# Performance work log

Measured on AMD Instinct MI355X. Metric: run time of the kernel, lower is better.

Reference implementation:

```python
import jax, jax.numpy as jnp
import numpy as np

IN_SIZE = 1024
CLASSES = 7
N = 50000
LN_EPS = 1e-5


def _chain(x, w, b, g, beta):
    # Linear -> (Dropout=identity at eval) -> LayerNorm -> GELU(exact erf)
    h = x @ w.T + b
    mu = jnp.mean(h, axis=-1, keepdims=True)
    var = jnp.var(h, axis=-1, keepdims=True)
    h = (h - mu) / jnp.sqrt(var + LN_EPS) * g + beta
    return jax.nn.gelu(h, approximate=False)


def setup_inputs() -> dict:
    key = jax.random.key(0)
    ks = jax.random.split(key, 16)
    d = IN_SIZE
    std = 1.0 / np.sqrt(d)
    inp = {
        "features": jax.random.normal(ks[0], (N, d), jnp.float32),
        "c": jax.random.normal(ks[1], (N, CLASSES), jnp.float32),
        "key_w": jax.random.uniform(ks[2], (d, d), jnp.float32, -std, std),
        "key_b": jax.random.uniform(ks[3], (d,), jnp.float32, -std, std),
        "key_g": jnp.ones((d,), jnp.float32),
        "key_beta": jnp.zeros((d,), jnp.float32),
        "query_w": jax.random.uniform(ks[4], (d, d), jnp.float32, -std, std),
        "query_b": jax.random.uniform(ks[5], (d,), jnp.float32, -std, std),
        "query_g": jnp.ones((d,), jnp.float32),
        "query_beta": jnp.zeros((d,), jnp.float32),
        "value_w": jax.random.uniform(ks[6], (d, d), jnp.float32, -std, std),
        "value_b": jax.random.uniform(ks[7], (d,), jnp.float32, -std, std),
        "value_g": jnp.ones((d,), jnp.float32),
        "value_beta": jnp.zeros((d,), jnp.float32),
        "head_w": jax.random.uniform(ks[8], (CLASSES, CLASSES, d), jnp.float32, -1.0 / np.sqrt(CLASSES * d), 1.0 / np.sqrt(CLASSES * d)),
        "head_b": jax.random.uniform(ks[9], (CLASSES,), jnp.float32, -1.0 / np.sqrt(CLASSES * d), 1.0 / np.sqrt(CLASSES * d)),
    }
    return inp


def reference(features, c, key_w, key_b, key_g, key_beta,
              query_w, query_b, query_g, query_beta,
              value_w, value_b, value_g, value_beta,
              head_w, head_b):
    K = _chain(features, key_w, key_b, key_g, key_beta)          # [N, d]
    V = _chain(K, value_w, value_b, value_g, value_beta)         # [N, d]
    Q = _chain(K, query_w, query_b, query_g, query_beta)         # [N, d]
    # critical (top-scoring) instance per class
    top_idx = jnp.argmax(c, axis=0)                              # [classes]
    m_feats = K[top_idx]                                         # [classes, d]
    q_max = _chain(m_feats, query_w, query_b, query_g, query_beta)  # [classes, d]
    A = Q @ q_max.T                                              # [N, classes]
    A = jax.nn.softmax(A / jnp.sqrt(jnp.float32(Q.shape[1])), axis=0)
    B = A.T @ V                                                  # [classes, d]
    # Conv1d(classes, classes, kernel_size=d) on [1, classes, d] -> full contraction
    C = jnp.einsum('ik,oik->o', B, head_w) + head_b              # [classes]
    C = C.reshape(1, -1)
    return (C, A, B.reshape(1, CLASSES, -1))
```

## Files before the change

kernel.cpp:

```cpp
#include <hip/hip_runtime.h>


typedef unsigned short u16;
typedef __attribute__((ext_vector_type(8))) short          bf16x8;
typedef __attribute__((ext_vector_type(8))) unsigned short u16x8;
typedef __attribute__((ext_vector_type(4))) unsigned short u16x4;
typedef __attribute__((ext_vector_type(4))) float          f32x4;

#define DDIM  1024
#define NROWS 50000
#define MP    50048
#define NCLS  7
#define MPD4  12512

__device__ __forceinline__ u16 f2bf(float f) {
  unsigned u = __float_as_uint(f);
  u = (u + 0x7FFFu + ((u >> 16) & 1u)) >> 16;
  return (u16)u;
}
__device__ __forceinline__ float bf2f(u16 h) {
  return __uint_as_float(((unsigned)h) << 16);
}
__device__ __forceinline__ float gelu(float x) {
  return 0.5f * x * (1.0f + erff(x * 0.70710678118654752f));
}

__device__ __forceinline__ void load16_lds(const u16* g, u16* l) {
  __builtin_amdgcn_global_load_lds(
      (const __attribute__((address_space(1))) unsigned int*)(const void*)g,
      (__attribute__((address_space(3))) unsigned int*)(void*)l, 16, 0, 0);
}

__global__ __launch_bounds__(256) void k_convert(const float* __restrict__ src,
                                                 u16* __restrict__ dst,
                                                 int rows_total, int rows_valid) {
  const size_t total = (size_t)rows_total * DDIM / 8;
  const size_t stride = (size_t)gridDim.x * blockDim.x;
  for (size_t i = (size_t)blockIdx.x * blockDim.x + threadIdx.x; i < total; i += stride) {
    const size_t e = i * 8;
    const int row = (int)(e >> 10);
    u16x8 o = {0, 0, 0, 0, 0, 0, 0, 0};
    if (row < rows_valid) {
      const float4* p = (const float4*)(src + e);
      float4 f0 = p[0], f1 = p[1];
      o[0] = f2bf(f0.x); o[1] = f2bf(f0.y); o[2] = f2bf(f0.z); o[3] = f2bf(f0.w);
      o[4] = f2bf(f1.x); o[5] = f2bf(f1.y); o[6] = f2bf(f1.z); o[7] = f2bf(f1.w);
    }
    *(u16x8*)(dst + e) = o;
  }
}

__global__ __launch_bounds__(256) void k_convw(const float* __restrict__ kw,
                                               const float* __restrict__ vw,
                                               const float* __restrict__ qw,
                                               u16* __restrict__ Wk,
                                               u16* __restrict__ Wvq) {
  const int w = blockIdx.x >> 7;
  const int b = blockIdx.x & 127;
  const float* src = (w == 0) ? kw : (w == 1) ? vw : qw;
  u16* dst = (w == 0) ? Wk : (Wvq + (size_t)(w - 1) * DDIM * DDIM);
  for (int i = b * 256 + threadIdx.x; i < DDIM * DDIM / 8; i += 128 * 256) {
    const float4* p = (const float4*)(src + (size_t)i * 8);
    float4 f0 = p[0], f1 = p[1];
    u16x8 o;
    o[0] = f2bf(f0.x); o[1] = f2bf(f0.y); o[2] = f2bf(f0.z); o[3] = f2bf(f0.w);
    o[4] = f2bf(f1.x); o[5] = f2bf(f1.y); o[6] = f2bf(f1.z); o[7] = f2bf(f1.w);
    *(u16x8*)(dst + (size_t)i * 8) = o;
  }
}

__global__ __launch_bounds__(256) void k_gemm_bt(const u16* __restrict__ A,
                                                 const u16* __restrict__ B,
                                                 u16* __restrict__ C,
                                                 int lnn, int ldc) {
  __shared__ __align__(16) u16 As[3][4096];
  __shared__ __align__(16) u16 Bs[3][4096];
  const int tid  = threadIdx.x;
  const int lane = tid & 63;
  const int cpx = gridDim.x >> 3;
  const int v   = (blockIdx.x & 7) * cpx + (blockIdx.x >> 3);
  const int m0 = (v >> lnn) * 128;
  const int n0 = (v & ((1 << lnn) - 1)) * 128;
  const int wid = tid >> 6;
  const int wr = (wid >> 1) * 64;
  const int wc = (wid & 1) * 64;

  const int rA = tid >> 2;
  const int cA = (((tid & 3) ^ ((rA >> 1) & 3)) << 3);
  const u16* Ap0 = A + (size_t)(m0 + rA) * DDIM + cA;
  const u16* Ap1 = Ap0 + (size_t)64 * DDIM;
  const u16* Bp0 = B + (size_t)(n0 + rA) * DDIM + cA;
  const u16* Bp1 = Bp0 + (size_t)64 * DDIM;
  const int wb8 = wid * 512;

  f32x4 acc[4][4] = {};
  const int fr = lane & 15;
  const int T  = lane >> 4;

#define STAGE_KT(KT, BUF) do { const int _ko = (KT) * 32;                      \
    load16_lds(Ap0 + _ko, &As[BUF][wb8]);                                      \
    load16_lds(Ap1 + _ko, &As[BUF][wb8 + 2048]);                               \
    load16_lds(Bp0 + _ko, &Bs[BUF][wb8]);                                      \
    load16_lds(Bp1 + _ko, &Bs[BUF][wb8 + 2048]); } while (0)

#define COMPUTE_KT(BUF) do {                                                   \
    const u16* _Ab = &As[BUF][0]; const u16* _Bb = &Bs[BUF][0];                \
    bf16x8 a[4], b[4];                                                         \
    _Pragma("unroll") for (int i = 0; i < 4; ++i) {                            \
      const int R = wr + i * 16 + fr;                                          \
      a[i] = *(const bf16x8*)&_Ab[R * 32 + ((T ^ ((R >> 1) & 3)) << 3)];       \
    }                                                                          \
    _Pragma("unroll") for (int j = 0; j < 4; ++j) {                            \
      const int R = wc + j * 16 + fr;                                          \
      b[j] = *(const bf16x8*)&_Bb[R * 32 + ((T ^ ((R >> 1) & 3)) << 3)];       \
    }                                                                          \
    _Pragma("unroll") for (int i = 0; i < 4; ++i)                              \
      _Pragma("unroll") for (int j = 0; j < 4; ++j)                            \
        acc[i][j] = __builtin_amdgcn_mfma_f32_16x16x32_bf16(a[i], b[j],        \
                                                            acc[i][j], 0, 0, 0); } while (0)

#define RBAR(N) asm volatile("s_waitcnt vmcnt(" #N ")\n\ts_barrier" ::: "memory")

  STAGE_KT(0, 0); STAGE_KT(1, 1);
  RBAR(4);
  for (int kt = 0; kt < 30; kt += 3) {
    STAGE_KT(kt + 2, 2); COMPUTE_KT(0); RBAR(4);
    STAGE_KT(kt + 3, 0); COMPUTE_KT(1); RBAR(4);
    STAGE_KT(kt + 4, 1); COMPUTE_KT(2); RBAR(4);
  }
  COMPUTE_KT(0);
  RBAR(0);
  COMPUTE_KT(1);
#undef STAGE_KT
#undef COMPUTE_KT
#undef RBAR

  const int orow = (lane >> 4) * 4;
  const int ocol = lane & 15;
#pragma unroll
  for (int i = 0; i < 4; ++i)
#pragma unroll
    for (int j = 0; j < 4; ++j) {
      const size_t base = (size_t)(m0 + wr + i * 16 + orow) * ldc + (n0 + wc + j * 16 + ocol);
#pragma unroll
      for (int r = 0; r < 4; ++r)
        C[base + (size_t)r * ldc] = f2bf(acc[i][j][r]);
    }
}

__global__ __launch_bounds__(256) void k_ln_k(const u16* __restrict__ h,
                                              const float* __restrict__ bias,
                                              const float* __restrict__ g,
                                              const float* __restrict__ beta,
                                              u16* __restrict__ out) {
  const int lane = threadIdx.x & 63;
  const int row = blockIdx.x * 4 + (threadIdx.x >> 6);
  const int c0 = lane * 8;
  u16x8* op0 = (u16x8*)(out + (size_t)row * DDIM + c0);
  u16x8* op1 = (u16x8*)(out + (size_t)row * DDIM + 512 + c0);
  if (row >= NROWS) {
    u16x8 z = {0, 0, 0, 0, 0, 0, 0, 0};
    *op0 = z; *op1 = z;
    return;
  }
  u16x8 h0 = *(const u16x8*)(h + (size_t)row * DDIM + c0);
  u16x8 h1 = *(const u16x8*)(h + (size_t)row * DDIM + 512 + c0);
  float4 a0 = *(const float4*)(bias + c0), a1 = *(const float4*)(bias + c0 + 4);
  float4 a2 = *(const float4*)(bias + 512 + c0), a3 = *(const float4*)(bias + 512 + c0 + 4);
  const float ba[8] = {a0.x, a0.y, a0.z, a0.w, a1.x, a1.y, a1.z, a1.w};
  const float bb[8] = {a2.x, a2.y, a2.z, a2.w, a3.x, a3.y, a3.z, a3.w};
  float v0[8], v1[8];
  float s1 = 0.f, s2 = 0.f;
#pragma unroll
  for (int e = 0; e < 8; ++e) {
    v0[e] = bf2f(h0[e]) + ba[e];
    v1[e] = bf2f(h1[e]) + bb[e];
    s1 += v0[e] + v1[e];
    s2 += v0[e] * v0[e] + v1[e] * v1[e];
  }
#pragma unroll
  for (int m = 1; m < 64; m <<= 1) {
    s1 += __shfl_xor(s1, m, 64);
    s2 += __shfl_xor(s2, m, 64);
  }
  const float mu = s1 * (1.0f / 1024.0f);
  const float var = s2 * (1.0f / 1024.0f) - mu * mu;
  const float rs = rsqrtf(var + 1e-5f);
  float4 g0 = *(const float4*)(g + c0), g1 = *(const float4*)(g + c0 + 4);
  float4 g2 = *(const float4*)(g + 512 + c0), g3 = *(const float4*)(g + 512 + c0 + 4);
  float4 t0 = *(const float4*)(beta + c0), t1 = *(const float4*)(beta + c0 + 4);
  float4 t2 = *(const float4*)(beta + 512 + c0), t3 = *(const float4*)(beta + 512 + c0 + 4);
  const float ga[8] = {g0.x, g0.y, g0.z, g0.w, g1.x, g1.y, g1.z, g1.w};
  const float gb[8] = {g2.x, g2.y, g2.z, g2.w, g3.x, g3.y, g3.z, g3.w};
  const float ta[8] = {t0.x, t0.y, t0.z, t0.w, t1.x, t1.y, t1.z, t1.w};
  const float tb[8] = {t2.x, t2.y, t2.z, t2.w, t3.x, t3.y, t3.z, t3.w};
  u16x8 o0, o1;
#pragma unroll
  for (int e = 0; e < 8; ++e) {
    o0[e] = f2bf(gelu((v0[e] - mu) * rs * ga[e] + ta[e]));
    o1[e] = f2bf(gelu((v1[e] - mu) * rs * gb[e] + tb[e]));
  }
  *op0 = o0; *op1 = o1;
}

__global__ __launch_bounds__(64) void k_qmax2(const float* __restrict__ argv,
                                              const int* __restrict__ argi,
                                              const u16* __restrict__ hvq,
                                              const float* __restrict__ qb,
                                              const float* __restrict__ qg,
                                              const float* __restrict__ qbeta,
                                              u16* __restrict__ qm) {
  const int j = blockIdx.x;
  const int lane = threadIdx.x;
  float bv = -3.4e38f; int bi = 0x7fffffff;
  for (int p = lane; p < 128; p += 64) {
    const float v = argv[p * NCLS + j];
    const int   i = argi[p * NCLS + j];
    if (v > bv || (v == bv && i < bi)) { bv = v; bi = i; }
  }
#pragma unroll
  for (int m = 1; m < 64; m <<= 1) {
    const float ov = __shfl_xor(bv, m, 64);
    const int   oi = __shfl_xor(bi, m, 64);
    if (ov > bv || (ov == bv && oi < bi)) { bv = ov; bi = oi; }
  }
  const int row = bi;
  const int c0 = lane * 8;
  const u16* hp = hvq + (size_t)row * 2048 + DDIM;
  u16x8 h0 = *(const u16x8*)(hp + c0);
  u16x8 h1 = *(const u16x8*)(hp + 512 + c0);
  float v0[8], v1[8];
  float s1 = 0.f, s2 = 0.f;
#pragma unroll
  for (int e = 0; e < 8; ++e) {
    v0[e] = bf2f(h0[e]) + qb[c0 + e];
    v1[e] = bf2f(h1[e]) + qb[512 + c0 + e];
    s1 += v0[e] + v1[e];
    s2 += v0[e] * v0[e] + v1[e] * v1[e];
  }
#pragma unroll
  for (int m = 1; m < 64; m <<= 1) {
    s1 += __shfl_xor(s1, m, 64);
    s2 += __shfl_xor(s2, m, 64);
  }
  const float mu = s1 * (1.0f / 1024.0f);
  const float var = s2 * (1.0f / 1024.0f) - mu * mu;
  const float rs = rsqrtf(var + 1e-5f);
  u16x8 o0, o1;
#pragma unroll
  for (int e = 0; e < 8; ++e) {
    o0[e] = f2bf(gelu((v0[e] - mu) * rs * qg[c0 + e] + qbeta[c0 + e]));
    o1[e] = f2bf(gelu((v1[e] - mu) * rs * qg[512 + c0 + e] + qbeta[512 + c0 + e]));
  }
  *(u16x8*)(qm + (size_t)j * DDIM + c0) = o0;
  *(u16x8*)(qm + (size_t)j * DDIM + 512 + c0) = o1;
}

__global__ __launch_bounds__(256) void k_ln_vq(const u16* __restrict__ h,
                                               const float* __restrict__ v_b,
                                               const float* __restrict__ v_g,
                                               const float* __restrict__ v_beta,
                                               const float* __restrict__ q_b,
                                               const float* __restrict__ q_g,
                                               const float* __restrict__ q_beta,
                                               const u16* __restrict__ qm,
                                               u16* __restrict__ V,
                                               float* __restrict__ logits) {
  __shared__ __align__(16) u16 sqm[NCLS * DDIM];
  const int tid = threadIdx.x;
  const int lane = tid & 63;
  const int half = (blockIdx.x >= MPD4) ? 1 : 0;
  const int rb = half ? (blockIdx.x - MPD4) : blockIdx.x;
  const int row = rb * 4 + (tid >> 6);
  if (half) {
    for (int i = tid; i < NCLS * DDIM / 8; i += 256)
      *(u16x8*)&sqm[i * 8] = *(const u16x8*)&qm[i * 8];
    __syncthreads();
  }
  if (row >= NROWS) return;
  const float* bias = half ? q_b : v_b;
  const float* gain = half ? q_g : v_g;
  const float* bet  = half ? q_beta : v_beta;
  const int c0 = lane * 8;
  const u16* hp = h + (size_t)row * 2048 + (size_t)half * DDIM;
  u16x8 h0 = *(const u16x8*)(hp + c0);
  u16x8 h1 = *(const u16x8*)(hp + 512 + c0);
  float4 a0 = *(const float4*)(bias + c0), a1 = *(const float4*)(bias + c0 + 4);
  float4 a2 = *(const float4*)(bias + 512 + c0), a3 = *(const float4*)(bias + 512 + c0 + 4);
  const float ba[8] = {a0.x, a0.y, a0.z, a0.w, a1.x, a1.y, a1.z, a1.w};
  const float bb[8] = {a2.x, a2.y, a2.z, a2.w, a3.x, a3.y, a3.z, a3.w};
  float v0[8], v1[8];
  float s1 = 0.f, s2 = 0.f;
#pragma unroll
  for (int e = 0; e < 8; ++e) {
    v0[e] = bf2f(h0[e]) + ba[e];
    v1[e] = bf2f(h1[e]) + bb[e];
    s1 += v0[e] + v1[e];
    s2 += v0[e] * v0[e] + v1[e] * v1[e];
  }
#pragma unroll
  for (int m = 1; m < 64; m <<= 1) {
    s1 += __shfl_xor(s1, m, 64);
    s2 += __shfl_xor(s2, m, 64);
  }
  const float mu = s1 * (1.0f / 1024.0f);
  const float var = s2 * (1.0f / 1024.0f) - mu * mu;
  const float rs = rsqrtf(var + 1e-5f);
  float4 g0 = *(const float4*)(gain + c0), g1 = *(const float4*)(gain + c0 + 4);
  float4 g2 = *(const float4*)(gain + 512 + c0), g3 = *(const float4*)(gain + 512 + c0 + 4);
  float4 t0 = *(const float4*)(bet + c0), t1 = *(const float4*)(bet + c0 + 4);
  float4 t2 = *(const float4*)(bet + 512 + c0), t3 = *(const float4*)(bet + 512 + c0 + 4);
  const float ga[8] = {g0.x, g0.y, g0.z, g0.w, g1.x, g1.y, g1.z, g1.w};
  const float gb[8] = {g2.x, g2.y, g2.z, g2.w, g3.x, g3.y, g3.z, g3.w};
  const float ta[8] = {t0.x, t0.y, t0.z, t0.w, t1.x, t1.y, t1.z, t1.w};
  const float tb[8] = {t2.x, t2.y, t2.z, t2.w, t3.x, t3.y, t3.z, t3.w};
  float y0[8], y1[8];
#pragma unroll
  for (int e = 0; e < 8; ++e) {
    y0[e] = gelu((v0[e] - mu) * rs * ga[e] + ta[e]);
    y1[e] = gelu((v1[e] - mu) * rs * gb[e] + tb[e]);
  }
  if (half == 0) {
    u16x8 o0, o1;
#pragma unroll
    for (int e = 0; e < 8; ++e) { o0[e] = f2bf(y0[e]); o1[e] = f2bf(y1[e]); }
    *(u16x8*)(V + (size_t)row * DDIM + c0) = o0;
    *(u16x8*)(V + (size_t)row * DDIM + 512 + c0) = o1;
  } else {
#pragma unroll
    for (int j = 0; j < NCLS; ++j) {
      u16x8 m0 = *(const u16x8*)&sqm[j * DDIM + c0];
      u16x8 m1 = *(const u16x8*)&sqm[j * DDIM + 512 + c0];
      float p = 0.f;
#pragma unroll
      for (int e = 0; e < 8; ++e) p += y0[e] * bf2f(m0[e]) + y1[e] * bf2f(m1[e]);
#pragma unroll
      for (int m = 1; m < 64; m <<= 1) p += __shfl_xor(p, m, 64);
      if (lane == 0) logits[(size_t)row * NCLS + j] = p * 0.03125f;
    }
  }
}

__global__ __launch_bounds__(256) void k_arg1(const float* __restrict__ c,
                                              float* __restrict__ pv,
                                              int* __restrict__ pi) {
  __shared__ float sv[256 * NCLS];
  __shared__ int   si[256 * NCLS];
  const int t = threadIdx.x;
  float bv[NCLS]; int bi[NCLS];
#pragma unroll
  for (int j = 0; j < NCLS; ++j) { bv[j] = -3.4e38f; bi[j] = 0x7fffffff; }
  for (int n = blockIdx.x * 256 + t; n < NROWS; n += 128 * 256) {
#pragma unroll
    for (int j = 0; j < NCLS; ++j) {
      const float v = c[(size_t)n * NCLS + j];
      if (v > bv[j]) { bv[j] = v; bi[j] = n; }
    }
  }
#pragma unroll
  for (int j = 0; j < NCLS; ++j) { sv[t * NCLS + j] = bv[j]; si[t * NCLS + j] = bi[j]; }
  __syncthreads();
  for (int s = 128; s > 0; s >>= 1) {
    if (t < s) {
#pragma unroll
      for (int j = 0; j < NCLS; ++j) {
        const float v2 = sv[(t + s) * NCLS + j]; const int i2 = si[(t + s) * NCLS + j];
        const float v1 = sv[t * NCLS + j];       const int i1 = si[t * NCLS + j];
        if (v2 > v1 || (v2 == v1 && i2 < i1)) { sv[t * NCLS + j] = v2; si[t * NCLS + j] = i2; }
      }
    }
    __syncthreads();
  }
  if (t < NCLS) { pv[blockIdx.x * NCLS + t] = sv[t]; pi[blockIdx.x * NCLS + t] = si[t]; }
}

__global__ __launch_bounds__(256) void k_cmax_part(const float* __restrict__ logits,
                                                   float* __restrict__ pout) {
  __shared__ float sm[256 * NCLS];
  const int tid = threadIdx.x;
  float m[NCLS];
#pragma unroll
  for (int j = 0; j < NCLS; ++j) m[j] = -3.4e38f;
  const size_t stride = (size_t)gridDim.x * 256;
  for (size_t n = (size_t)blockIdx.x * 256 + tid; n < NROWS; n += stride)
#pragma unroll
    for (int j = 0; j < NCLS; ++j) m[j] = fmaxf(m[j], logits[n * NCLS + j]);
#pragma unroll
  for (int j = 0; j < NCLS; ++j) sm[tid * NCLS + j] = m[j];
  __syncthreads();
  for (int s = 128; s > 0; s >>= 1) {
    if (tid < s)
#pragma unroll
      for (int j = 0; j < NCLS; ++j)
        sm[tid * NCLS + j] = fmaxf(sm[tid * NCLS + j], sm[(tid + s) * NCLS + j]);
    __syncthreads();
  }
  if (tid < NCLS) pout[blockIdx.x * NCLS + tid] = sm[tid];
}

__global__ __launch_bounds__(256) void k_csum_part(const float* __restrict__ logits,
                                                   const float* __restrict__ Pmax,
                                                   float* __restrict__ pout) {
  __shared__ float sm[256 * NCLS];
  __shared__ float sM[NCLS];
  const int tid = threadIdx.x;
  if (tid < NCLS) {
    float m = -3.4e38f;
    for (int b = 0; b < 128; ++b) m = fmaxf(m, Pmax[b * NCLS + tid]);
    sM[tid] = m;
  }
  __syncthreads();
  float s[NCLS];
#pragma unroll
  for (int j = 0; j < NCLS; ++j) s[j] = 0.f;
  const size_t stride = (size_t)gridDim.x * 256;
  for (size_t n = (size_t)blockIdx.x * 256 + tid; n < NROWS; n += stride)
#pragma unroll
    for (int j = 0; j < NCLS; ++j) s[j] += expf(logits[n * NCLS + j] - sM[j]);
#pragma unroll
  for (int j = 0; j < NCLS; ++j) sm[tid * NCLS + j] = s[j];
  __syncthreads();
  for (int st = 128; st > 0; st >>= 1) {
    if (tid < st)
#pragma unroll
      for (int j = 0; j < NCLS; ++j) sm[tid * NCLS + j] += sm[(tid + st) * NCLS + j];
    __syncthreads();
  }
  if (tid < NCLS) pout[blockIdx.x * NCLS + tid] = sm[tid];
}

__global__ __launch_bounds__(256) void k_bpart(const float* __restrict__ logits,
                                               const float* __restrict__ Pmax,
                                               const float* __restrict__ Psum,
                                               const u16* __restrict__ V,
                                               float* __restrict__ Aout,
                                               float* __restrict__ Pb) {
  __shared__ float sA[98 * NCLS];
  __shared__ float sM[NCLS], sR[NCLS];
  const int t = threadIdx.x;
  if (t < NCLS) {
    float m = -3.4e38f;
    for (int b = 0; b < 128; ++b) m = fmaxf(m, Pmax[b * NCLS + t]);
    float s = 0.f;
    for (int b = 0; b < 128; ++b) s += Psum[b * NCLS + t];
    sM[t] = m; sR[t] = 1.0f / s;
  }
  __syncthreads();
  const int n0 = blockIdx.x * 98;
  int cnt = NROWS - n0;
  cnt = cnt < 0 ? 0 : (cnt > 98 ? 98 : cnt);
  for (int idx = t; idx < cnt * NCLS; idx += 256) {
    const int j = idx % NCLS;
    const float a = expf(logits[(size_t)n0 * NCLS + idx] - sM[j]) * sR[j];
    sA[idx] = a;
    Aout[(size_t)n0 * NCLS + idx] = a;
  }
  __syncthreads();
  float acc[NCLS][4] = {};
  for (int r = 0; r < cnt; ++r) {
    u16x4 vv = *(const u16x4*)&V[(size_t)(n0 + r) * DDIM + t * 4];
    const float f0 = bf2f(vv[0]), f1 = bf2f(vv[1]), f2 = bf2f(vv[2]), f3 = bf2f(vv[3]);
#pragma unroll
    for (int j = 0; j < NCLS; ++j) {
      const float a = sA[r * NCLS + j];
      acc[j][0] += a * f0; acc[j][1] += a * f1; acc[j][2] += a * f2; acc[j][3] += a * f3;
    }
  }
#pragma unroll
  for (int j = 0; j < NCLS; ++j) {
    f32x4 o = {acc[j][0], acc[j][1], acc[j][2], acc[j][3]};
    *(f32x4*)&Pb[((size_t)blockIdx.x * NCLS + j) * DDIM + t * 4] = o;
  }
}

__global__ void k_bred(const float* __restrict__ Pb, float* __restrict__ Bout) {
  const int idx = blockIdx.x * 256 + threadIdx.x;
  if (idx >= NCLS * DDIM) return;
  float s = 0.f;
  for (int p = 0; p < 512; ++p) s += Pb[(size_t)p * NCLS * DDIM + idx];
  Bout[idx] = s;
}

__global__ __launch_bounds__(256) void k_head(const float* __restrict__ Bmat,
                                              const float* __restrict__ hw,
                                              const float* __restrict__ hb,
                                              float* __restrict__ Cout) {
  const int o = blockIdx.x, t = threadIdx.x;
  float p = 0.f;
  for (int idx = t; idx < NCLS * DDIM; idx += 256)
    p += Bmat[idx] * hw[(size_t)o * NCLS * DDIM + idx];
#pragma unroll
  for (int m = 1; m < 64; m <<= 1) p += __shfl_xor(p, m, 64);
  __shared__ float w[4];
  if ((t & 63) == 0) w[t >> 6] = p;
  __syncthreads();
  if (t == 0) Cout[o] = w[0] + w[1] + w[2] + w[3] + hb[o];
}

extern "C" void kernel_launch(void* const* d_in, const int* in_sizes, int n_in,
                              void* d_out, int out_size, void* d_ws, size_t ws_size,
                              hipStream_t stream) {
  const float* features   = (const float*)d_in[0];
  const float* c_in       = (const float*)d_in[1];
  const float* key_w      = (const float*)d_in[2];
  const float* key_b      = (const float*)d_in[3];
  const float* key_g      = (const float*)d_in[4];
  const float* key_beta   = (const float*)d_in[5];
  const float* query_w    = (const float*)d_in[6];
  const float* query_b    = (const float*)d_in[7];
  const float* query_g    = (const float*)d_in[8];
  const float* query_beta = (const float*)d_in[9];
  const float* value_w    = (const float*)d_in[10];
  const float* value_b    = (const float*)d_in[11];
  const float* value_g    = (const float*)d_in[12];
  const float* value_beta = (const float*)d_in[13];
  const float* head_w     = (const float*)d_in[14];
  const float* head_b     = (const float*)d_in[15];

  char* ws = (char*)d_ws;
  const size_t SZB = (size_t)MP * DDIM * 2;
  u16* Xb   = (u16*)ws;
  u16* HbVQ = Xb;
  u16* HbK  = (u16*)(ws + SZB);
  u16* Kb   = (u16*)(ws + 2 * SZB);
  u16* Vb   = Kb;
  size_t off = 3 * SZB;
  u16* Wk  = (u16*)(ws + off); off += (size_t)DDIM * DDIM * 2;
  u16* Wvq = (u16*)(ws + off); off += (size_t)2 * DDIM * DDIM * 2;
  float* logits = (float*)(ws + off); off += ((size_t)NROWS * NCLS * 4 + 255) & ~(size_t)255;
  float* Pb  = (float*)(ws + off); off += (size_t)512 * NCLS * DDIM * 4;
  u16* qm    = (u16*)(ws + off); off += ((size_t)NCLS * DDIM * 2 + 255) & ~(size_t)255;
  float* Pmax = (float*)(ws + off); off += ((size_t)128 * NCLS * 4 + 255) & ~(size_t)255;
  float* Psum = (float*)(ws + off); off += ((size_t)128 * NCLS * 4 + 255) & ~(size_t)255;
  float* argv = (float*)(ws + off); off += ((size_t)128 * NCLS * 4 + 255) & ~(size_t)255;
  int*   argi = (int*)  (ws + off); off += ((size_t)128 * NCLS * 4 + 255) & ~(size_t)255;

  float* Cout = (float*)d_out;
  float* Aout = Cout + NCLS;
  float* Bout = Aout + (size_t)NROWS * NCLS;

  k_arg1<<<128, 256, 0, stream>>>(c_in, argv, argi);
  k_convert<<<2048, 256, 0, stream>>>(features, Xb, MP, NROWS);
  k_convw<<<384, 256, 0, stream>>>(key_w, value_w, query_w, Wk, Wvq);

  k_gemm_bt<<<3128, 256, 0, stream>>>(Xb, Wk, HbK, 3, 1024);
  k_ln_k<<<MPD4, 256, 0, stream>>>(HbK, key_b, key_g, key_beta, Kb);

  k_gemm_bt<<<6256, 256, 0, stream>>>(Kb, Wvq, HbVQ, 4, 2048);
  k_qmax2<<<NCLS, 64, 0, stream>>>(argv, argi, HbVQ, query_b, query_g, query_beta, qm);
  k_ln_vq<<<2 * MPD4, 256, 0, stream>>>(HbVQ, value_b, value_g, value_beta,
                                        query_b, query_g, query_beta, qm, Vb, logits);

  k_cmax_part<<<128, 256, 0, stream>>>(logits, Pmax);
  k_csum_part<<<128, 256, 0, stream>>>(logits, Pmax, Psum);

  k_bpart<<<512, 256, 0, stream>>>(logits, Pmax, Psum, Vb, Aout, Pb);
  k_bred<<<28, 256, 0, stream>>>(Pb, Bout);
  k_head<<<NCLS, 256, 0, stream>>>(Bout, head_w, head_b, Cout);
}
```

Before: 826.7 us.

## Fuse fp32->bf16 feature conversion into GEMM, single-buffer GEMM, merge softmax partials

Removes the separate feature-conversion kernel by loading fp32 features directly inside the first GEMM and converting them to bf16 in registers before writing to LDS. The GEMM is also simplified from a triple-buffered async pipeline to a single-buffered loop with two barriers per k-step, which likely loses load/compute overlap for both GEMMs. The softmax max and sum partial kernels are merged into one kernel using per-block local maxima, and the rescaling moves into the consumer. The workspace layout changes so the bf16 features buffer is no longer needed.

```diff
diff --git a/kernel.cpp b/kernel.cpp
--- a/kernel.cpp
+++ b/kernel.cpp
@@ -29,25 +29,6 @@
   __builtin_amdgcn_global_load_lds(
       (const __attribute__((address_space(1))) unsigned int*)(const void*)g,
       (__attribute__((address_space(3))) unsigned int*)(void*)l, 16, 0, 0);
-}
-
-__global__ __launch_bounds__(256) void k_convert(const float* __restrict__ src,
-                                                 u16* __restrict__ dst,
-                                                 int rows_total, int rows_valid) {
-  const size_t total = (size_t)rows_total * DDIM / 8;
-  const size_t stride = (size_t)gridDim.x * blockDim.x;
-  for (size_t i = (size_t)blockIdx.x * blockDim.x + threadIdx.x; i < total; i += stride) {
-    const size_t e = i * 8;
-    const int row = (int)(e >> 10);
-    u16x8 o = {0, 0, 0, 0, 0, 0, 0, 0};
-    if (row < rows_valid) {
-      const float4* p = (const float4*)(src + e);
-      float4 f0 = p[0], f1 = p[1];
-      o[0] = f2bf(f0.x); o[1] = f2bf(f0.y); o[2] = f2bf(f0.z); o[3] = f2bf(f0.w);
-      o[4] = f2bf(f1.x); o[5] = f2bf(f1.y); o[6] = f2bf(f1.z); o[7] = f2bf(f1.w);
-    }
-    *(u16x8*)(dst + e) = o;
-  }
 }
 
 __global__ __launch_bounds__(256) void k_convw(const float* __restrict__ kw,
@@ -69,12 +50,14 @@
   }
 }
 
-__global__ __launch_bounds__(256) void k_gemm_bt(const u16* __restrict__ A,
-                                                 const u16* __restrict__ B,
-                                                 u16* __restrict__ C,
-                                                 int lnn, int ldc) {
-  __shared__ __align__(16) u16 As[3][4096];
-  __shared__ __align__(16) u16 Bs[3][4096];
+template<int AFP32>
+__global__ __launch_bounds__(256) void k_gemm(const float* __restrict__ Af,
+                                              const u16* __restrict__ Ab,
+                                              const u16* __restrict__ B,
+                                              u16* __restrict__ C,
+                                              int lnn, int ldc) {
+  __shared__ __align__(16) u16 As[128 * 32];
+  __shared__ __align__(16) u16 Bs[128 * 32];
   const int tid  = threadIdx.x;
   const int lane = tid & 63;
   const int cpx = gridDim.x >> 3;
@@ -86,54 +69,78 @@
   const int wc = (wid & 1) * 64;
 
   const int rA = tid >> 2;
-  const int cA = (((tid & 3) ^ ((rA >> 1) & 3)) << 3);
-  const u16* Ap0 = A + (size_t)(m0 + rA) * DDIM + cA;
-  const u16* Ap1 = Ap0 + (size_t)64 * DDIM;
+  const int slotl = tid & 3;
+  const int swz = (rA >> 1) & 3;
+  const int cA = ((slotl ^ swz) << 3);
   const u16* Bp0 = B + (size_t)(n0 + rA) * DDIM + cA;
   const u16* Bp1 = Bp0 + (size_t)64 * DDIM;
-  const int wb8 = wid * 512;
+  const u16* Ap0 = nullptr; const u16* Ap1 = nullptr;
+  const float* Fp0 = nullptr; const float* Fp1 = nullptr;
+  bool av0 = false, av1 = false;
+  if (AFP32) {
+    av0 = (m0 + rA) < NROWS;
+    av1 = (m0 + rA + 64) < NROWS;
+    Fp0 = Af + (size_t)(m0 + rA) * DDIM + slotl * 8;
+    Fp1 = Fp0 + (size_t)64 * DDIM;
+  } else {
+    Ap0 = Ab + (size_t)(m0 + rA) * DDIM + cA;
+    Ap1 = Ap0 + (size_t)64 * DDIM;
+  }
+  const int wbase = wid * 64;
+  u16* AsD0 = &As[(wbase)       * 8];
+  u16* AsD1 = &As[(wbase + 256) * 8];
+  u16* BsD0 = &Bs[(wbase)       * 8];
+  u16* BsD1 = &Bs[(wbase + 256) * 8];
+  u16* AsW0 = &As[rA * 32 + (cA ^ 0)];
+  u16* AsW1 = &As[(rA + 64) * 32 + cA];
 
   f32x4 acc[4][4] = {};
   const int fr = lane & 15;
   const int T  = lane >> 4;
 
-#define STAGE_KT(KT, BUF) do { const int _ko = (KT) * 32;                      \
-    load16_lds(Ap0 + _ko, &As[BUF][wb8]);                                      \
-    load16_lds(Ap1 + _ko, &As[BUF][wb8 + 2048]);                               \
-    load16_lds(Bp0 + _ko, &Bs[BUF][wb8]);                                      \
-    load16_lds(Bp1 + _ko, &Bs[BUF][wb8 + 2048]); } while (0)
-
-#define COMPUTE_KT(BUF) do {                                                   \
-    const u16* _Ab = &As[BUF][0]; const u16* _Bb = &Bs[BUF][0];                \
-    bf16x8 a[4], b[4];                                                         \
-    _Pragma("unroll") for (int i = 0; i < 4; ++i) {                            \
-      const int R = wr + i * 16 + fr;                                          \
-      a[i] = *(const bf16x8*)&_Ab[R * 32 + ((T ^ ((R >> 1) & 3)) << 3)];       \
-    }                                                                          \
-    _Pragma("unroll") for (int j = 0; j < 4; ++j) {                            \
-      const int R = wc + j * 16 + fr;                                          \
-      b[j] = *(const bf16x8*)&_Bb[R * 32 + ((T ^ ((R >> 1) & 3)) << 3)];       \
-    }                                                                          \
-    _Pragma("unroll") for (int i = 0; i < 4; ++i)                              \
-      _Pragma("unroll") for (int j = 0; j < 4; ++j)                            \
-        acc[i][j] = __builtin_amdgcn_mfma_f32_16x16x32_bf16(a[i], b[j],        \
-                                                            acc[i][j], 0, 0, 0); } while (0)
-
-#define RBAR(N) asm volatile("s_waitcnt vmcnt(" #N ")\n\ts_barrier" ::: "memory")
-
-  STAGE_KT(0, 0); STAGE_KT(1, 1);
-  RBAR(4);
-  for (int kt = 0; kt < 30; kt += 3) {
-    STAGE_KT(kt + 2, 2); COMPUTE_KT(0); RBAR(4);
-    STAGE_KT(kt + 3, 0); COMPUTE_KT(1); RBAR(4);
-    STAGE_KT(kt + 4, 1); COMPUTE_KT(2); RBAR(4);
-  }
-  COMPUTE_KT(0);
-  RBAR(0);
-  COMPUTE_KT(1);
-#undef STAGE_KT
-#undef COMPUTE_KT
-#undef RBAR
+  for (int k0 = 0; k0 < DDIM; k0 += 32) {
+    float4 fa0, fb0, fa1, fb1;
+    if (AFP32) {
+      if (av0) { fa0 = *(const float4*)(Fp0 + k0); fb0 = *(const float4*)(Fp0 + k0 + 4); }
+      if (av1) { fa1 = *(const float4*)(Fp1 + k0); fb1 = *(const float4*)(Fp1 + k0 + 4); }
+    }
+    __syncthreads();
+    if (AFP32) {
+      u16x8 o0 = {0,0,0,0,0,0,0,0}, o1 = {0,0,0,0,0,0,0,0};
+      if (av0) {
+        o0[0]=f2bf(fa0.x); o0[1]=f2bf(fa0.y); o0[2]=f2bf(fa0.z); o0[3]=f2bf(fa0.w);
+        o0[4]=f2bf(fb0.x); o0[5]=f2bf(fb0.y); o0[6]=f2bf(fb0.z); o0[7]=f2bf(fb0.w);
+      }
+      if (av1) {
+        o1[0]=f2bf(fa1.x); o1[1]=f2bf(fa1.y); o1[2]=f2bf(fa1.z); o1[3]=f2bf(fa1.w);
+        o1[4]=f2bf(fb1.x); o1[5]=f2bf(fb1.y); o1[6]=f2bf(fb1.z); o1[7]=f2bf(fb1.w);
+      }
+      *(u16x8*)AsW0 = o0;
+      *(u16x8*)AsW1 = o1;
+    } else {
+      load16_lds(Ap0 + k0, AsD0);
+      load16_lds(Ap1 + k0, AsD1);
+    }
+    load16_lds(Bp0 + k0, BsD0);
+    load16_lds(Bp1 + k0, BsD1);
+    __syncthreads();
+    bf16x8 a[4], b[4];
+#pragma unroll
+    for (int i = 0; i < 4; ++i) {
+      const int R = wr + i * 16 + fr;
+      a[i] = *(const bf16x8*)&As[R * 32 + ((T ^ ((R >> 1) & 3)) << 3)];
+    }
+#pragma unroll
+    for (int j = 0; j < 4; ++j) {
+      const int R = wc + j * 16 + fr;
+      b[j] = *(const bf16x8*)&Bs[R * 32 + ((T ^ ((R >> 1) & 3)) << 3)];
+    }
+#pragma unroll
+    for (int i = 0; i < 4; ++i)
+#pragma unroll
+      for (int j = 0; j < 4; ++j)
+        acc[i][j] = __builtin_amdgcn_mfma_f32_16x16x32_bf16(a[i], b[j], acc[i][j], 0, 0, 0);
+  }
 
   const int orow = (lane >> 4) * 4;
   const int ocol = lane & 15;
@@ -374,64 +381,52 @@
   if (t < NCLS) { pv[blockIdx.x * NCLS + t] = sv[t]; pi[blockIdx.x * NCLS + t] = si[t]; }
 }
 
-__global__ __launch_bounds__(256) void k_cmax_part(const float* __restrict__ logits,
-                                                   float* __restrict__ pout) {
+__global__ __launch_bounds__(256) void k_softpart(const float* __restrict__ logits,
+                                                  float* __restrict__ Pm,
+                                                  float* __restrict__ Ps) {
   __shared__ float sm[256 * NCLS];
-  const int tid = threadIdx.x;
+  const int t = threadIdx.x;
   float m[NCLS];
 #pragma unroll
   for (int j = 0; j < NCLS; ++j) m[j] = -3.4e38f;
-  const size_t stride = (size_t)gridDim.x * 256;
-  for (size_t n = (size_t)blockIdx.x * 256 + tid; n < NROWS; n += stride)
-#pragma unroll
-    for (int j = 0; j < NCLS; ++j) m[j] = fmaxf(m[j], logits[n * NCLS + j]);
-#pragma unroll
-  for (int j = 0; j < NCLS; ++j) sm[tid * NCLS + j] = m[j];
+  for (int n = blockIdx.x * 256 + t; n < NROWS; n += 128 * 256)
+#pragma unroll
+    for (int j = 0; j < NCLS; ++j) m[j] = fmaxf(m[j], logits[(size_t)n * NCLS + j]);
+#pragma unroll
+  for (int j = 0; j < NCLS; ++j) sm[t * NCLS + j] = m[j];
   __syncthreads();
   for (int s = 128; s > 0; s >>= 1) {
-    if (tid < s)
+    if (t < s)
 #pragma unroll
       for (int j = 0; j < NCLS; ++j)
-        sm[tid * NCLS + j] = fmaxf(sm[tid * NCLS + j], sm[(tid + s) * NCLS + j]);
+        sm[t * NCLS + j] = fmaxf(sm[t * NCLS + j], sm[(t + s) * NCLS + j]);
     __syncthreads();
   }
-  if (tid < NCLS) pout[blockIdx.x * NCLS + tid] = sm[tid];
-}
-
-__global__ __launch_bounds__(256) void k_csum_part(const float* __restrict__ logits,
-                                                   const float* __restrict__ Pmax,
-                                                   float* __restrict__ pout) {
-  __shared__ float sm[256 * NCLS];
-  __shared__ float sM[NCLS];
-  const int tid = threadIdx.x;
-  if (tid < NCLS) {
-    float m = -3.4e38f;
-    for (int b = 0; b < 128; ++b) m = fmaxf(m, Pmax[b * NCLS + tid]);
-    sM[tid] = m;
-  }
+  float mloc[NCLS];
+#pragma unroll
+  for (int j = 0; j < NCLS; ++j) mloc[j] = sm[j];
   __syncthreads();
   float s[NCLS];
 #pragma unroll
   for (int j = 0; j < NCLS; ++j) s[j] = 0.f;
-  const size_t stride = (size_t)gridDim.x * 256;
-  for (size_t n = (size_t)blockIdx.x * 256 + tid; n < NROWS; n += stride)
-#pragma unroll
-    for (int j = 0; j < NCLS; ++j) s[j] += expf(logits[n * NCLS + j] - sM[j]);
-#pragma unroll
-  for (int j = 0; j < NCLS; ++j) sm[tid * NCLS + j] = s[j];
+  for (int n = blockIdx.x * 256 + t; n < NROWS; n += 128 * 256)
+#pragma unroll
+    for (int j = 0; j < NCLS; ++j) s[j] += expf(logits[(size_t)n * NCLS + j] - mloc[j]);
+#pragma unroll
+  for (int j = 0; j < NCLS; ++j) sm[t * NCLS + j] = s[j];
   __syncthreads();
   for (int st = 128; st > 0; st >>= 1) {
-    if (tid < st)
-#pragma unroll
-      for (int j = 0; j < NCLS; ++j) sm[tid * NCLS + j] += sm[(tid + st) * NCLS + j];
+    if (t < st)
+#pragma unroll
+      for (int j = 0; j < NCLS; ++j) sm[t * NCLS + j] += sm[(t + st) * NCLS + j];
     __syncthreads();
   }
-  if (tid < NCLS) pout[blockIdx.x * NCLS + tid] = sm[tid];
+  if (t < NCLS) { Pm[blockIdx.x * NCLS + t] = mloc[t]; Ps[blockIdx.x * NCLS + t] = sm[t]; }
 }
 
 __global__ __launch_bounds__(256) void k_bpart(const float* __restrict__ logits,
-                                               const float* __restrict__ Pmax,
-                                               const float* __restrict__ Psum,
+                                               const float* __restrict__ Pm,
+                                               const float* __restrict__ Ps,
                                                const u16* __restrict__ V,
                                                float* __restrict__ Aout,
                                                float* __restrict__ Pb) {
@@ -439,11 +434,11 @@
   __shared__ float sM[NCLS], sR[NCLS];
   const int t = threadIdx.x;
   if (t < NCLS) {
-    float m = -3.4e38f;
-    for (int b = 0; b < 128; ++b) m = fmaxf(m, Pmax[b * NCLS + t]);
-    float s = 0.f;
-    for (int b = 0; b < 128; ++b) s += Psum[b * NCLS + t];
-    sM[t] = m; sR[t] = 1.0f / s;
+    float M = -3.4e38f;
+    for (int b = 0; b < 128; ++b) M = fmaxf(M, Pm[b * NCLS + t]);
+    float S = 0.f;
+    for (int b = 0; b < 128; ++b) S += Ps[b * NCLS + t] * expf(Pm[b * NCLS + t] - M);
+    sM[t] = M; sR[t] = 1.0f / S;
   }
   __syncthreads();
   const int n0 = blockIdx.x * 98;
@@ -519,12 +514,11 @@
 
   char* ws = (char*)d_ws;
   const size_t SZB = (size_t)MP * DDIM * 2;
-  u16* Xb   = (u16*)ws;
-  u16* HbVQ = Xb;
-  u16* HbK  = (u16*)(ws + SZB);
-  u16* Kb   = (u16*)(ws + 2 * SZB);
+  u16* HbK  = (u16*)ws;
+  u16* Kb   = (u16*)(ws + SZB);
+  u16* HbVQ = (u16*)(ws + 2 * SZB);
   u16* Vb   = Kb;
-  size_t off = 3 * SZB;
+  size_t off = 4 * SZB;
   u16* Wk  = (u16*)(ws + off); off += (size_t)DDIM * DDIM * 2;
   u16* Wvq = (u16*)(ws + off); off += (size_t)2 * DDIM * DDIM * 2;
   float* logits = (float*)(ws + off); off += ((size_t)NROWS * NCLS * 4 + 255) & ~(size_t)255;
@@ -540,19 +534,17 @@
   float* Bout = Aout + (size_t)NROWS * NCLS;
 
   k_arg1<<<128, 256, 0, stream>>>(c_in, argv, argi);
-  k_convert<<<2048, 256, 0, stream>>>(features, Xb, MP, NROWS);
   k_convw<<<384, 256, 0, stream>>>(key_w, value_w, query_w, Wk, Wvq);
 
-  k_gemm_bt<<<3128, 256, 0, stream>>>(Xb, Wk, HbK, 3, 1024);
+  k_gemm<1><<<3128, 256, 0, stream>>>(features, nullptr, Wk, HbK, 3, 1024);
   k_ln_k<<<MPD4, 256, 0, stream>>>(HbK, key_b, key_g, key_beta, Kb);
 
-  k_gemm_bt<<<6256, 256, 0, stream>>>(Kb, Wvq, HbVQ, 4, 2048);
+  k_gemm<0><<<6256, 256, 0, stream>>>(nullptr, Kb, Wvq, HbVQ, 4, 2048);
   k_qmax2<<<NCLS, 64, 0, stream>>>(argv, argi, HbVQ, query_b, query_g, query_beta, qm);
   k_ln_vq<<<2 * MPD4, 256, 0, stream>>>(HbVQ, value_b, value_g, value_beta,
                                         query_b, query_g, query_beta, qm, Vb, logits);
 
-  k_cmax_part<<<128, 256, 0, stream>>>(logits, Pmax);
-  k_csum_part<<<128, 256, 0, stream>>>(logits, Pmax, Psum);
+  k_softpart<<<128, 256, 0, stream>>>(logits, Pmax, Psum);
 
   k_bpart<<<512, 256, 0, stream>>>(logits, Pmax, Psum, Vb, Aout, Pb);
   k_bred<<<28, 256, 0, stream>>>(Pb, Bout);
```

New measurement: 746.2 us. -9.7%, faster.
